# Optimization experiments

Measured on AMD Instinct MI355X. Metric: run time of the kernel, lower is better.

## Reference

```python
import jax, jax.numpy as jnp
import numpy as np
import math

D_MODEL = 1024
N_HEADS = 16
D_HEAD = D_MODEL // N_HEADS
D_FF = 4 * D_MODEL
EPS = 1e-5


def layer_norm(x, gamma, beta):
    mu = jnp.mean(x, axis=-1, keepdims=True)
    var = jnp.var(x, axis=-1, keepdims=True)
    return (x - mu) * jax.lax.rsqrt(var + EPS) * gamma + beta


def setup_inputs() -> dict:
    key = jax.random.key(0)
    ks = jax.random.split(key, 8)
    B, C, D = 32, 256, D_MODEL
    s = 0.02
    return {
        "X": jax.random.normal(ks[0], (B, C, D), dtype=jnp.float32),
        "W_qkv": jax.random.normal(ks[1], (D, 3 * D), dtype=jnp.float32) * s,
        "b_qkv": jnp.zeros((3 * D,), dtype=jnp.float32),
        "W_proj": jax.random.normal(ks[2], (D, D), dtype=jnp.float32) * s,
        "b_proj": jnp.zeros((D,), dtype=jnp.float32),
        "g1": jnp.ones((D,), dtype=jnp.float32),
        "beta1": jnp.zeros((D,), dtype=jnp.float32),
        "g2": jnp.ones((D,), dtype=jnp.float32),
        "beta2": jnp.zeros((D,), dtype=jnp.float32),
        "W_ff1": jax.random.normal(ks[3], (D, D_FF), dtype=jnp.float32) * s,
        "b_ff1": jnp.zeros((D_FF,), dtype=jnp.float32),
        "W_ff2": jax.random.normal(ks[4], (D_FF, D), dtype=jnp.float32) * s,
        "b_ff2": jnp.zeros((D,), dtype=jnp.float32),
    }


def reference(X, W_qkv, b_qkv, W_proj, b_proj, g1, beta1, g2, beta2,
              W_ff1, b_ff1, W_ff2, b_ff2):
    B, C, D = X.shape
    H, Dh = N_HEADS, D_HEAD
    scale = 1.0 / math.sqrt(Dh)

    Xn = layer_norm(X, g1, beta1)
    qkv = Xn @ W_qkv + b_qkv                       # [B, C, 3D]
    q, k, v = jnp.split(qkv, 3, axis=-1)
    # split heads -> [B, H, C, Dh]
    sh = lambda t: t.reshape(B, C, H, Dh).transpose(0, 2, 1, 3)
    q, k, v = sh(q), sh(k), sh(v)

    scores = jnp.einsum("bhcd,bhkd->bhck", q, k) * scale  # [B, H, C, C]
    attn = jax.nn.softmax(scores, axis=-1)
    ctx = jnp.einsum("bhck,bhkd->bhcd", attn, v)           # [B, H, C, Dh]
    ctx = ctx.transpose(0, 2, 1, 3).reshape(B, C, D)

    X1 = X + (ctx @ W_proj + b_proj)
    X2n = layer_norm(X1, g2, beta2)
    h = jax.nn.gelu(X2n @ W_ff1 + b_ff1, approximate=False)
    X_out = X1 + (h @ W_ff2 + b_ff2)
    A = attn.mean(axis=1)                                   # [B, C, C]
    return (X_out, A)
```

## Files before the change

### kernel.cpp

```cpp
#include <hip/hip_runtime.h>
#include <cstdint>
#include <cstddef>

typedef short bf16x8 __attribute__((ext_vector_type(8)));
typedef float f32x4 __attribute__((ext_vector_type(4)));
typedef unsigned short u16;
typedef u16 u16x8 __attribute__((ext_vector_type(8)));

#define GLD16(gptr, lptr)                                                            \
  __builtin_amdgcn_global_load_lds((const __attribute__((address_space(1))) void*)(gptr), \
                                   (__attribute__((address_space(3))) void*)(lptr), 16, 0, 0)

__device__ __forceinline__ u16 f2bf(float f) {
  union { float f; unsigned u; } v; v.f = f;
  unsigned r = v.u + 0x7FFF + ((v.u >> 16) & 1);
  return (u16)(r >> 16);
}
__device__ __forceinline__ float bf2f(u16 h) {
  union { unsigned u; float f; } v; v.u = ((unsigned)h) << 16;
  return v.f;
}

template <int N> __device__ __forceinline__ void vmwait() {
  if constexpr (N == 0) asm volatile("s_waitcnt vmcnt(0)" ::: "memory");
  else if constexpr (N == 6) asm volatile("s_waitcnt vmcnt(6)" ::: "memory");
  else asm volatile("s_waitcnt vmcnt(8)" ::: "memory");
}

__device__ __forceinline__ bf16x8 lds_read_sw64(const u16* base, int row, int col) {
  int byt = row * 128 + col * 2;
  byt ^= (row & 7) << 4;
  return *(const bf16x8*)((const char*)base + byt);
}

__global__ __launch_bounds__(256) void transpose_cast(const float* __restrict__ in,
                                                      u16* __restrict__ out, int R, int C) {
  __shared__ float tile[32][33];
  const int tx = threadIdx.x, ty = threadIdx.y;
  const int c0 = blockIdx.x * 32, r0 = blockIdx.y * 32;
#pragma unroll
  for (int i = 0; i < 32; i += 8)
    tile[ty + i][tx] = in[(size_t)(r0 + ty + i) * C + c0 + tx];
  __syncthreads();
#pragma unroll
  for (int i = 0; i < 32; i += 8)
    out[(size_t)(c0 + ty + i) * R + r0 + tx] = f2bf(tile[tx][ty + i]);
}

__global__ __launch_bounds__(256) void layernorm_bf16(const float* __restrict__ X,
                                                      const float* __restrict__ g,
                                                      const float* __restrict__ be,
                                                      u16* __restrict__ out) {
  const int row = blockIdx.x, t = threadIdx.x;
  const int lane = t & 63, wave = t >> 6;
  const float* x = X + (size_t)row * 1024;
  __shared__ float part[4];
  float v[4]; float s = 0.f;
#pragma unroll
  for (int i = 0; i < 4; ++i) { v[i] = x[t + i * 256]; s += v[i]; }
#pragma unroll
  for (int o = 32; o >= 1; o >>= 1) s += __shfl_xor(s, o);
  if (lane == 0) part[wave] = s;
  __syncthreads();
  const float mu = (part[0] + part[1] + part[2] + part[3]) * (1.f / 1024.f);
  float d2 = 0.f;
#pragma unroll
  for (int i = 0; i < 4; ++i) { float d = v[i] - mu; d2 += d * d; }
#pragma unroll
  for (int o = 32; o >= 1; o >>= 1) d2 += __shfl_xor(d2, o);
  __syncthreads();
  if (lane == 0) part[wave] = d2;
  __syncthreads();
  const float var = (part[0] + part[1] + part[2] + part[3]) * (1.f / 1024.f);
  const float rstd = rsqrtf(var + 1e-5f);
#pragma unroll
  for (int i = 0; i < 4; ++i) {
    const int c = t + i * 256;
    out[(size_t)row * 1024 + c] = f2bf((v[i] - mu) * rstd * g[c] + be[c]);
  }
}

template <int EPI>
__global__ __launch_bounds__(512, 2) void gemm_pipe(const u16* __restrict__ A,
                                                    const u16* __restrict__ Bt,
                                                    const float* __restrict__ bias,
                                                    const float* __restrict__ res,
                                                    float* __restrict__ outf,
                                                    u16* __restrict__ outb,
                                                    int M, int N, int K) {
  constexpr int MF = 8, NF = 2;
  constexpr int AT = 256 * 64, BT = 128 * 64;
  __shared__ u16 lds[2 * (AT + BT)];

  const int t = threadIdx.x, lane = t & 63, wave = t >> 6;
  const int wm = wave >> 2, wn = wave & 3;
  const int l15 = lane & 15, l16 = lane >> 4;

  const int lb = (blockIdx.x & 7) * ((int)gridDim.x >> 3) + ((int)blockIdx.x >> 3);
  const int NBN = N >> 7;
  const int bm = (lb / NBN) * 256, bn = (lb % NBN) * 128;

  const u16* aptr[4];
  const u16* bptr[2];
#pragma unroll
  for (int is = 0; is < 4; ++is) {
    int Lb = is * 8192 + t * 16;
    int x = (Lb ^ ((Lb >> 3) & 0x70)) >> 1;
    aptr[is] = A + (size_t)(bm + (x >> 6)) * K + (x & 63);
  }
#pragma unroll
  for (int is = 0; is < 2; ++is) {
    int Lb = is * 8192 + t * 16;
    int x = (Lb ^ ((Lb >> 3) & 0x70)) >> 1;
    bptr[is] = Bt + (size_t)(bn + (x >> 6)) * K + (x & 63);
  }

  auto stage = [&](int p) {
    const int ko = p * 64;
    char* ab = (char*)lds + (p & 1) * (AT * 2) + t * 16;
    char* bb = (char*)lds + 4 * AT + (p & 1) * (BT * 2) + t * 16;
#pragma unroll
    for (int is = 0; is < 4; ++is) GLD16(aptr[is] + ko, ab + is * 8192);
#pragma unroll
    for (int is = 0; is < 2; ++is) GLD16(bptr[is] + ko, bb + is * 8192);
  };
  stage(0); stage(1);

  const int rx = (l15 & 7) << 4;
  const int co0 = (l16 * 16) ^ rx;
  const int co1 = (64 + l16 * 16) ^ rx;

  f32x4 acc[MF][NF] = {};
  const int nkt = K >> 6;

#pragma unroll 1
  for (int kt = 0; kt < nkt; ++kt) {
    if (kt < nkt - 1) vmwait<6>(); else vmwait<0>();
    __builtin_amdgcn_s_barrier();

    const char* Ab = (const char*)lds + (kt & 1) * (AT * 2);
    const char* Bb = (const char*)lds + 4 * AT + (kt & 1) * (BT * 2);
    bf16x8 af[MF][2], bfr[NF][2];
#pragma unroll
    for (int n = 0; n < NF; ++n) {
      const int rb = (wn * NF * 16 + n * 16 + l15) * 128;
      bfr[n][0] = *(const bf16x8*)(Bb + rb + co0);
      bfr[n][1] = *(const bf16x8*)(Bb + rb + co1);
    }
#pragma unroll
    for (int m = 0; m < MF; ++m) {
      const int ra = (wm * MF * 16 + m * 16 + l15) * 128;
      af[m][0] = *(const bf16x8*)(Ab + ra + co0);
      af[m][1] = *(const bf16x8*)(Ab + ra + co1);
    }
    asm volatile("s_waitcnt lgkmcnt(0)" ::: "memory");
    __builtin_amdgcn_sched_barrier(0);
    __builtin_amdgcn_s_barrier();

    if (kt + 2 < nkt) stage(kt + 2);
    __builtin_amdgcn_sched_barrier(0);

    __builtin_amdgcn_s_setprio(1);
#pragma unroll
    for (int m = 0; m < MF; ++m)
#pragma unroll
      for (int n = 0; n < NF; ++n) {
        acc[m][n] = __builtin_amdgcn_mfma_f32_16x16x32_bf16(af[m][0], bfr[n][0], acc[m][n], 0, 0, 0);
        acc[m][n] = __builtin_amdgcn_mfma_f32_16x16x32_bf16(af[m][1], bfr[n][1], acc[m][n], 0, 0, 0);
      }
    __builtin_amdgcn_s_setprio(0);
  }

  const int r0 = l16 * 4;
#pragma unroll
  for (int m = 0; m < MF; ++m) {
#pragma unroll
    for (int n = 0; n < NF; ++n) {
      const int col = bn + wn * 32 + n * 16 + l15;
      const float bv = bias[col];
#pragma unroll
      for (int r = 0; r < 4; ++r) {
        const int row = bm + wm * 128 + m * 16 + r0 + r;
        const float v = acc[m][n][r] + bv;
        const size_t o = (size_t)row * N + col;
        if (EPI == 0) {
          outb[o] = f2bf(v);
        } else if (EPI == 1) {
          outf[o] = res[o] + v;
        } else {
          const float u = 0.7978845608f * (v + 0.044715f * v * v * v);
          const float e = __expf(2.f * u);
          const float th = 1.f - 2.f / (1.f + e);
          outb[o] = f2bf(0.5f * v * (1.f + th));
        }
      }
    }
  }
}

__global__ __launch_bounds__(256) void attn_scores(const u16* __restrict__ qkv,
                                                   u16* __restrict__ probs) {
  __shared__ u16 Ks[256 * 64];
  __shared__ u16 Qs[64 * 64];
  const int t = threadIdx.x, lane = t & 63, wave = t >> 6;
  const int qb = blockIdx.x * 64, h = blockIdx.y, b = blockIdx.z;
  const size_t row0 = (size_t)b * 256 * 3072;

#pragma unroll
  for (int is = 0; is < 8; ++is) {
    int L = (is * 2048 + t * 8) * 2;
    int x = (L ^ ((L >> 3) & 0x70)) >> 1;
    int kk = x >> 6, d = x & 63;
    const u16* gp = qkv + row0 + (size_t)kk * 3072 + 1024 + h * 64 + d;
    GLD16(gp, (char*)Ks + is * 4096 + wave * 1024);
  }
#pragma unroll
  for (int is = 0; is < 2; ++is) {
    int L = (is * 2048 + t * 8) * 2;
    int x = (L ^ ((L >> 3) & 0x70)) >> 1;
    int q = x >> 6, d = x & 63;
    const u16* gp = qkv + row0 + (size_t)(qb + q) * 3072 + h * 64 + d;
    GLD16(gp, (char*)Qs + is * 4096 + wave * 1024);
  }
  __syncthreads();

  f32x4 acc[16] = {};
  bf16x8 aq[2];
#pragma unroll
  for (int ks = 0; ks < 2; ++ks)
    aq[ks] = lds_read_sw64(Qs, wave * 16 + (lane & 15), ks * 32 + (lane >> 4) * 8);
#pragma unroll
  for (int nf = 0; nf < 16; ++nf) {
#pragma unroll
    for (int ks = 0; ks < 2; ++ks) {
      bf16x8 bk = lds_read_sw64(Ks, nf * 16 + (lane & 15), ks * 32 + (lane >> 4) * 8);
      acc[nf] = __builtin_amdgcn_mfma_f32_16x16x32_bf16(aq[ks], bk, acc[nf], 0, 0, 0);
    }
  }

  const int r0 = (lane >> 4) * 4, cc = lane & 15;
  const float sc = 0.125f;
#pragma unroll
  for (int r = 0; r < 4; ++r) {
    float mx = -1e30f;
#pragma unroll
    for (int nf = 0; nf < 16; ++nf) mx = fmaxf(mx, acc[nf][r]);
#pragma unroll
    for (int o = 8; o >= 1; o >>= 1) mx = fmaxf(mx, __shfl_xor(mx, o));
    float s = 0.f;
#pragma unroll
    for (int nf = 0; nf < 16; ++nf) {
      float e = __expf((acc[nf][r] - mx) * sc);
      acc[nf][r] = e; s += e;
    }
#pragma unroll
    for (int o = 8; o >= 1; o >>= 1) s += __shfl_xor(s, o);
    const float rinv = 1.f / s;
    const int qrow = qb + wave * 16 + r0 + r;
    u16* prow = probs + (size_t)((b * 16 + h) * 256 + qrow) * 256;
#pragma unroll
    for (int nf = 0; nf < 16; ++nf)
      prow[nf * 16 + cc] = f2bf(acc[nf][r] * rinv);
  }
}

__global__ __launch_bounds__(256) void amean(const u16* __restrict__ probs,
                                             float* __restrict__ A) {
  const int bq = blockIdx.x;
  const int b = bq >> 8, q = bq & 255;
  const int t = threadIdx.x;
  float s = 0.f;
#pragma unroll
  for (int h = 0; h < 16; ++h)
    s += bf2f(probs[(size_t)((b * 16 + h) * 256 + q) * 256 + t]);
  A[(size_t)bq * 256 + t] = s * (1.f / 16.f);
}

__global__ __launch_bounds__(256) void attn_pv(const u16* __restrict__ qkv,
                                               const u16* __restrict__ probs,
                                               u16* __restrict__ ctx) {
  __shared__ u16 Vs[64 * 256];
  const int t = threadIdx.x, lane = t & 63, wave = t >> 6;
  const int h = blockIdx.x, b = blockIdx.y;

#pragma unroll
  for (int p = 0; p < 8; ++p) {
    int idx = p * 2048 + t * 8;
    int kk = idx >> 6, d0 = idx & 63;
    u16x8 vv = *(const u16x8*)(qkv + (size_t)(b * 256 + kk) * 3072 + 2048 + h * 64 + d0);
#pragma unroll
    for (int j = 0; j < 8; ++j) {
      int d = d0 + j;
      int byt = (d * 512 + kk * 2) ^ ((d & 7) << 4);
      *(u16*)((char*)Vs + byt) = vv[j];
    }
  }
  __syncthreads();

  f32x4 acc[4][4] = {};
  const u16* Pb = probs + (size_t)((b * 16 + h) * 256) * 256;
  const int cc = lane & 15, kg = (lane >> 4) * 8;
#pragma unroll
  for (int kt = 0; kt < 8; ++kt) {
    bf16x8 a[4], v[4];
#pragma unroll
    for (int m = 0; m < 4; ++m)
      a[m] = *(const bf16x8*)(Pb + (size_t)(wave * 64 + m * 16 + cc) * 256 + kt * 32 + kg);
#pragma unroll
    for (int n = 0; n < 4; ++n) {
      int d = n * 16 + cc;
      int kk = kt * 32 + kg;
      int byt = (d * 512 + kk * 2) ^ ((d & 7) << 4);
      v[n] = *(const bf16x8*)((const char*)Vs + byt);
    }
#pragma unroll
    for (int m = 0; m < 4; ++m)
#pragma unroll
      for (int n = 0; n < 4; ++n)
        acc[m][n] = __builtin_amdgcn_mfma_f32_16x16x32_bf16(a[m], v[n], acc[m][n], 0, 0, 0);
  }

  const int r0 = (lane >> 4) * 4;
#pragma unroll
  for (int m = 0; m < 4; ++m) {
    const int q = wave * 64 + m * 16 + r0;
#pragma unroll
    for (int n = 0; n < 4; ++n) {
      const int col = h * 64 + n * 16 + cc;
#pragma unroll
      for (int r = 0; r < 4; ++r)
        ctx[(size_t)(b * 256 + q + r) * 1024 + col] = f2bf(acc[m][n][r]);
    }
  }
}

extern "C" void kernel_launch(void* const* d_in, const int* in_sizes, int n_in,
                              void* d_out, int out_size, void* d_ws, size_t ws_size,
                              hipStream_t stream) {
  const float* X      = (const float*)d_in[0];
  const float* W_qkv  = (const float*)d_in[1];
  const float* b_qkv  = (const float*)d_in[2];
  const float* W_proj = (const float*)d_in[3];
  const float* b_proj = (const float*)d_in[4];
  const float* g1     = (const float*)d_in[5];
  const float* beta1  = (const float*)d_in[6];
  const float* g2     = (const float*)d_in[7];
  const float* beta2  = (const float*)d_in[8];
  const float* W_ff1  = (const float*)d_in[9];
  const float* b_ff1  = (const float*)d_in[10];
  const float* W_ff2  = (const float*)d_in[11];
  const float* b_ff2  = (const float*)d_in[12];

  float* Xout = (float*)d_out;
  float* Aout = (float*)d_out + 8388608;

  char* ws = (char*)d_ws;
  const size_t MB = 1u << 20;
  u16* xn    = (u16*)(ws + 0);
  u16* wqkv  = (u16*)(ws + 16 * MB);
  u16* wproj = (u16*)(ws + 22 * MB);
  u16* wff1  = (u16*)(ws + 24 * MB);
  u16* wff2  = (u16*)(ws + 32 * MB);
  u16* qkv   = (u16*)(ws + 40 * MB);
  u16* probs = (u16*)(ws + 88 * MB);
  u16* hbuf  = probs;
  float* x1  = (float*)(ws + 152 * MB);
  u16* ctx   = xn;
  u16* x1n   = xn;

  const dim3 tb(32, 8);
  transpose_cast<<<dim3(96, 32),  tb, 0, stream>>>(W_qkv,  wqkv, 1024, 3072);
  transpose_cast<<<dim3(32, 32),  tb, 0, stream>>>(W_proj, wproj, 1024, 1024);
  transpose_cast<<<dim3(128, 32), tb, 0, stream>>>(W_ff1,  wff1, 1024, 4096);
  transpose_cast<<<dim3(32, 128), tb, 0, stream>>>(W_ff2,  wff2, 4096, 1024);

  layernorm_bf16<<<8192, 256, 0, stream>>>(X, g1, beta1, xn);

  gemm_pipe<0><<<768, 512, 0, stream>>>(xn, wqkv, b_qkv, nullptr, nullptr, qkv,
                                        8192, 3072, 1024);

  attn_scores<<<dim3(4, 16, 32), 256, 0, stream>>>(qkv, probs);
  amean<<<8192, 256, 0, stream>>>(probs, Aout);
  attn_pv<<<dim3(16, 32), 256, 0, stream>>>(qkv, probs, ctx);

  gemm_pipe<1><<<256, 512, 0, stream>>>(ctx, wproj, b_proj, X, x1, nullptr,
                                        8192, 1024, 1024);

  layernorm_bf16<<<8192, 256, 0, stream>>>(x1, g2, beta2, x1n);

  gemm_pipe<2><<<1024, 512, 0, stream>>>(x1n, wff1, b_ff1, nullptr, nullptr, hbuf,
                                         8192, 4096, 1024);

  gemm_pipe<1><<<256, 512, 0, stream>>>(hbuf, wff2, b_ff2, x1, Xout, nullptr,
                                        8192, 1024, 4096);
}
```

Before: 380.9 us.

## Replace double-buffered GEMM with three-stage LDS ring and 64x64 wave tiles

Rewrites the bf16 GEMM to use a three-slot LDS ring so the next prefetch can be issued right after a single barrier per k-step, removing the second barrier and the lgkmcnt wait. Wave tiling changes from 128x32 to 64x64 per wave, cutting LDS fragment reads per MFMA. The larger LDS footprint forces one block per CU, trading occupancy for deeper in-block pipelining.

```diff
diff --git a/kernel.cpp b/kernel.cpp
--- a/kernel.cpp
+++ b/kernel.cpp
@@ -24,7 +24,7 @@
 template <int N> __device__ __forceinline__ void vmwait() {
   if constexpr (N == 0) asm volatile("s_waitcnt vmcnt(0)" ::: "memory");
   else if constexpr (N == 6) asm volatile("s_waitcnt vmcnt(6)" ::: "memory");
-  else asm volatile("s_waitcnt vmcnt(8)" ::: "memory");
+  else asm volatile("s_waitcnt vmcnt(12)" ::: "memory");
 }
 
 __device__ __forceinline__ bf16x8 lds_read_sw64(const u16* base, int row, int col) {
@@ -81,19 +81,19 @@
 }
 
 template <int EPI>
-__global__ __launch_bounds__(512, 2) void gemm_pipe(const u16* __restrict__ A,
-                                                    const u16* __restrict__ Bt,
-                                                    const float* __restrict__ bias,
-                                                    const float* __restrict__ res,
-                                                    float* __restrict__ outf,
-                                                    u16* __restrict__ outb,
-                                                    int M, int N, int K) {
-  constexpr int MF = 8, NF = 2;
-  constexpr int AT = 256 * 64, BT = 128 * 64;
-  __shared__ u16 lds[2 * (AT + BT)];
+__global__ __launch_bounds__(512, 1) void gemm_ring3(const u16* __restrict__ A,
+                                                     const u16* __restrict__ Bt,
+                                                     const float* __restrict__ bias,
+                                                     const float* __restrict__ res,
+                                                     float* __restrict__ outf,
+                                                     u16* __restrict__ outb,
+                                                     int M, int N, int K) {
+  constexpr int ABYT = 256 * 128;
+  constexpr int BBYT = 128 * 128;
+  __shared__ __attribute__((aligned(16))) char lds[3 * (ABYT + BBYT)];
 
   const int t = threadIdx.x, lane = t & 63, wave = t >> 6;
-  const int wm = wave >> 2, wn = wave & 3;
+  const int wm = wave >> 1, wn = wave & 1;
   const int l15 = lane & 15, l16 = lane >> 4;
 
   const int lb = (blockIdx.x & 7) * ((int)gridDim.x >> 3) + ((int)blockIdx.x >> 3);
@@ -103,84 +103,81 @@
   const u16* aptr[4];
   const u16* bptr[2];
 #pragma unroll
-  for (int is = 0; is < 4; ++is) {
-    int Lb = is * 8192 + t * 16;
+  for (int c = 0; c < 4; ++c) {
+    int Lb = c * 8192 + t * 16;
     int x = (Lb ^ ((Lb >> 3) & 0x70)) >> 1;
-    aptr[is] = A + (size_t)(bm + (x >> 6)) * K + (x & 63);
-  }
-#pragma unroll
-  for (int is = 0; is < 2; ++is) {
-    int Lb = is * 8192 + t * 16;
+    aptr[c] = A + (size_t)(bm + (x >> 6)) * K + (x & 63);
+  }
+#pragma unroll
+  for (int c = 0; c < 2; ++c) {
+    int Lb = c * 8192 + t * 16;
     int x = (Lb ^ ((Lb >> 3) & 0x70)) >> 1;
-    bptr[is] = Bt + (size_t)(bn + (x >> 6)) * K + (x & 63);
+    bptr[c] = Bt + (size_t)(bn + (x >> 6)) * K + (x & 63);
   }
 
   auto stage = [&](int p) {
     const int ko = p * 64;
-    char* ab = (char*)lds + (p & 1) * (AT * 2) + t * 16;
-    char* bb = (char*)lds + 4 * AT + (p & 1) * (BT * 2) + t * 16;
-#pragma unroll
-    for (int is = 0; is < 4; ++is) GLD16(aptr[is] + ko, ab + is * 8192);
-#pragma unroll
-    for (int is = 0; is < 2; ++is) GLD16(bptr[is] + ko, bb + is * 8192);
+    const int s = p % 3;
+    char* ab = lds + s * ABYT + t * 16;
+    char* bb = lds + 3 * ABYT + s * BBYT + t * 16;
+#pragma unroll
+    for (int c = 0; c < 4; ++c) GLD16(aptr[c] + ko, ab + c * 8192);
+#pragma unroll
+    for (int c = 0; c < 2; ++c) GLD16(bptr[c] + ko, bb + c * 8192);
   };
   stage(0); stage(1);
 
-  const int rx = (l15 & 7) << 4;
-  const int co0 = (l16 * 16) ^ rx;
-  const int co1 = (64 + l16 * 16) ^ rx;
-
-  f32x4 acc[MF][NF] = {};
+  const int rxA = ((wm * 64 + l15) & 7) << 4;
+  const int co0 = l16 * 16, co1 = 64 + l16 * 16;
+
+  f32x4 acc[4][4] = {};
   const int nkt = K >> 6;
 
 #pragma unroll 1
   for (int kt = 0; kt < nkt; ++kt) {
     if (kt < nkt - 1) vmwait<6>(); else vmwait<0>();
-    __builtin_amdgcn_s_barrier();
-
-    const char* Ab = (const char*)lds + (kt & 1) * (AT * 2);
-    const char* Bb = (const char*)lds + 4 * AT + (kt & 1) * (BT * 2);
-    bf16x8 af[MF][2], bfr[NF][2];
-#pragma unroll
-    for (int n = 0; n < NF; ++n) {
-      const int rb = (wn * NF * 16 + n * 16 + l15) * 128;
-      bfr[n][0] = *(const bf16x8*)(Bb + rb + co0);
-      bfr[n][1] = *(const bf16x8*)(Bb + rb + co1);
-    }
-#pragma unroll
-    for (int m = 0; m < MF; ++m) {
-      const int ra = (wm * MF * 16 + m * 16 + l15) * 128;
-      af[m][0] = *(const bf16x8*)(Ab + ra + co0);
-      af[m][1] = *(const bf16x8*)(Ab + ra + co1);
-    }
-    asm volatile("s_waitcnt lgkmcnt(0)" ::: "memory");
-    __builtin_amdgcn_sched_barrier(0);
-    __builtin_amdgcn_s_barrier();
-
+    asm volatile("s_barrier" ::: "memory");
     if (kt + 2 < nkt) stage(kt + 2);
-    __builtin_amdgcn_sched_barrier(0);
-
+
+    const int s = kt % 3;
+    const char* ab = lds + s * ABYT;
+    const char* bb = lds + 3 * ABYT + s * BBYT;
+    bf16x8 a[4][2], b[4][2];
+#pragma unroll
+    for (int m = 0; m < 4; ++m) {
+      const int r = wm * 64 + m * 16 + l15;
+      const int rb = r * 128, sw = (r & 7) << 4;
+      a[m][0] = *(const bf16x8*)(ab + rb + (co0 ^ sw));
+      a[m][1] = *(const bf16x8*)(ab + rb + (co1 ^ sw));
+    }
+#pragma unroll
+    for (int n = 0; n < 4; ++n) {
+      const int r = wn * 64 + n * 16 + l15;
+      const int rb = r * 128, sw = (r & 7) << 4;
+      b[n][0] = *(const bf16x8*)(bb + rb + (co0 ^ sw));
+      b[n][1] = *(const bf16x8*)(bb + rb + (co1 ^ sw));
+    }
     __builtin_amdgcn_s_setprio(1);
 #pragma unroll
-    for (int m = 0; m < MF; ++m)
-#pragma unroll
-      for (int n = 0; n < NF; ++n) {
-        acc[m][n] = __builtin_amdgcn_mfma_f32_16x16x32_bf16(af[m][0], bfr[n][0], acc[m][n], 0, 0, 0);
-        acc[m][n] = __builtin_amdgcn_mfma_f32_16x16x32_bf16(af[m][1], bfr[n][1], acc[m][n], 0, 0, 0);
-      }
+    for (int ks = 0; ks < 2; ++ks)
+#pragma unroll
+      for (int m = 0; m < 4; ++m)
+#pragma unroll
+        for (int n = 0; n < 4; ++n)
+          acc[m][n] = __builtin_amdgcn_mfma_f32_16x16x32_bf16(a[m][ks], b[n][ks], acc[m][n], 0, 0, 0);
     __builtin_amdgcn_s_setprio(0);
   }
 
   const int r0 = l16 * 4;
 #pragma unroll
-  for (int m = 0; m < MF; ++m) {
-#pragma unroll
-    for (int n = 0; n < NF; ++n) {
-      const int col = bn + wn * 32 + n * 16 + l15;
+  for (int m = 0; m < 4; ++m) {
+#pragma unroll
+    for (int n = 0; n < 4; ++n) {
+      const int col = bn + wn * 64 + n * 16 + l15;
       const float bv = bias[col];
 #pragma unroll
       for (int r = 0; r < 4; ++r) {
-        const int row = bm + wm * 128 + m * 16 + r0 + r;
+        const int row = bm + wm * 64 + m * 16 + r0 + r;
         const float v = acc[m][n][r] + bv;
         const size_t o = (size_t)row * N + col;
         if (EPI == 0) {
@@ -376,21 +373,21 @@
 
   layernorm_bf16<<<8192, 256, 0, stream>>>(X, g1, beta1, xn);
 
-  gemm_pipe<0><<<768, 512, 0, stream>>>(xn, wqkv, b_qkv, nullptr, nullptr, qkv,
-                                        8192, 3072, 1024);
+  gemm_ring3<0><<<768, 512, 0, stream>>>(xn, wqkv, b_qkv, nullptr, nullptr, qkv,
+                                         8192, 3072, 1024);
 
   attn_scores<<<dim3(4, 16, 32), 256, 0, stream>>>(qkv, probs);
   amean<<<8192, 256, 0, stream>>>(probs, Aout);
   attn_pv<<<dim3(16, 32), 256, 0, stream>>>(qkv, probs, ctx);
 
-  gemm_pipe<1><<<256, 512, 0, stream>>>(ctx, wproj, b_proj, X, x1, nullptr,
-                                        8192, 1024, 1024);
+  gemm_ring3<1><<<256, 512, 0, stream>>>(ctx, wproj, b_proj, X, x1, nullptr,
+                                         8192, 1024, 1024);
 
   layernorm_bf16<<<8192, 256, 0, stream>>>(x1, g2, beta2, x1n);
 
-  gemm_pipe<2><<<1024, 512, 0, stream>>>(x1n, wff1, b_ff1, nullptr, nullptr, hbuf,
-                                         8192, 4096, 1024);
-
-  gemm_pipe<1><<<256, 512, 0, stream>>>(hbuf, wff2, b_ff2, x1, Xout, nullptr,
-                                        8192, 1024, 4096);
-}
+  gemm_ring3<2><<<1024, 512, 0, stream>>>(x1n, wff1, b_ff1, nullptr, nullptr, hbuf,
+                                          8192, 4096, 1024);
+
+  gemm_ring3<1><<<256, 512, 0, stream>>>(hbuf, wff2, b_ff2, x1, Xout, nullptr,
+                                         8192, 1024, 4096);
+}
```

Measured after the change: 375.8 us. No clear change (-1.4%).
